# Performance work log

Hardware: AMD Instinct MI355X
Metric: run time of the kernel (lower is better)

The kernel has to match this reference:

```python
import jax, jax.numpy as jnp
import numpy as np

TEMPERATURE = 0.1
EPS = 1e-12  # matches torch F.normalize default eps


def setup_inputs() -> dict:
    key = jax.random.key(0)
    k1, k2 = jax.random.split(key)
    B, D = 4096, 512
    features1 = jax.random.normal(k1, (B, D), dtype=jnp.float32)
    features2 = jax.random.normal(k2, (B, D), dtype=jnp.float32)
    return {"features1": features1, "features2": features2}


def _l2_normalize(x, axis=1):
    norm = jnp.linalg.norm(x, axis=axis, keepdims=True)
    return x / jnp.maximum(norm, EPS)


def reference(features1, features2):
    B = features1.shape[0]
    f1 = _l2_normalize(features1)
    f2 = _l2_normalize(features2)
    features = jnp.concatenate([f1, f2], axis=0)  # (2B, D)
    sim = jnp.matmul(features, features.T) / TEMPERATURE  # (2B, 2B)
    # mask self-similarity on the diagonal with -inf
    diag = jnp.eye(2 * B, dtype=bool)
    sim = jnp.where(diag, -jnp.inf, sim)
    # positive pair labels: row i pairs with i+B (first half) / i-B (second half)
    labels = jnp.concatenate([jnp.arange(B) + B, jnp.arange(B)], axis=0)
    log_probs = jax.nn.log_softmax(sim, axis=-1)  # (2B, 2B)
    nll = -jnp.take_along_axis(log_probs, labels[:, None], axis=1)[:, 0]
    return jnp.mean(nll)
```

## Files before the change

kernel.cpp:

```cpp
#include <hip/hip_runtime.h>

#define NROWS 8192
#define HALF_N 4096
#define DIM 512
#define INV_T 10.0f
#define NRB 64
#define NBLOCKS 2080

typedef __attribute__((ext_vector_type(4))) float f32x4;
typedef __attribute__((ext_vector_type(2))) long long2v;

__device__ __forceinline__ void async16(const void* g, void* l) {
  __builtin_amdgcn_global_load_lds(
      (const __attribute__((address_space(1))) unsigned int*)g,
      (__attribute__((address_space(3))) unsigned int*)l, 16, 0, 0);
}

__global__ __launch_bounds__(256) void norm_cast_k(
    const float* __restrict__ f1, const float* __restrict__ f2,
    unsigned char* __restrict__ Fn, float* __restrict__ rowsum,
    float* __restrict__ out) {
  int wave = threadIdx.x >> 6;
  int lane = threadIdx.x & 63;
  int row = blockIdx.x * 4 + wave;
  const float* src = (row < HALF_N) ? (f1 + (size_t)row * DIM)
                                    : (f2 + (size_t)(row - HALF_N) * DIM);
  const float4* p = reinterpret_cast<const float4*>(src + lane * 8);
  float4 v0 = p[0];
  float4 v1 = p[1];
  float ss = v0.x*v0.x + v0.y*v0.y + v0.z*v0.z + v0.w*v0.w
           + v1.x*v1.x + v1.y*v1.y + v1.z*v1.z + v1.w*v1.w;
  #pragma unroll
  for (int off = 1; off < 64; off <<= 1) ss += __shfl_xor(ss, off);
  float scale = 1.0f / fmaxf(sqrtf(ss), 1e-12f);
  int lo = __builtin_amdgcn_cvt_pk_fp8_f32(v0.x * scale, v0.y * scale, 0, false);
  lo = __builtin_amdgcn_cvt_pk_fp8_f32(v0.z * scale, v0.w * scale, lo, true);
  int hi = __builtin_amdgcn_cvt_pk_fp8_f32(v1.x * scale, v1.y * scale, 0, false);
  hi = __builtin_amdgcn_cvt_pk_fp8_f32(v1.z * scale, v1.w * scale, hi, true);
  int u = lane & 7;
  int g = lane >> 3;
  int pos = 2 * (u & 3) + (u >> 2);
  *reinterpret_cast<int2*>(Fn + (size_t)row * DIM + g * 64 + pos * 8) =
      make_int2(lo, hi);
  if (lane == 0) rowsum[row] = 0.0f;
  if (blockIdx.x == 0 && threadIdx.x == 0) out[0] = 0.0f;
}

__global__ __launch_bounds__(256, 4) void sym_gemm_k(
    const unsigned char* __restrict__ Fn, float* __restrict__ rowsum,
    float* __restrict__ pairsim) {
  int bx = blockIdx.x;
  int gbx = (bx & 7) * (NBLOCKS / 8) + (bx >> 3);
  int rb = 0, rem = gbx;
  while (rem >= NRB - rb) { rem -= NRB - rb; ++rb; }
  const int cb = rb + rem;
  const int row0 = rb * 128, col0 = cb * 128;

  const int tid = threadIdx.x;
  const int wave = tid >> 6;
  const int lane = tid & 63;
  const int quad = lane >> 4;
  const int colid = lane & 15;
  const int wr0 = (wave >> 1) * 64;
  const int wc0 = (wave & 1) * 64;

  __shared__ __align__(16) unsigned char Alds[128 * 64];
  __shared__ __align__(16) unsigned char Blds[128 * 64];
  __shared__ float redrow[128];
  __shared__ float redcol[128];

  if (tid < 128) { redrow[tid] = 0.0f; redcol[tid] = 0.0f; }

  const unsigned char* srcA[2]; const unsigned char* srcB[2];
  unsigned char* dstA[2]; unsigned char* dstB[2];
  #pragma unroll
  for (int seg = 0; seg < 2; ++seg) {
    int inst = wave + seg * 4;
    int r = inst * 16 + (lane >> 2);
    int c = (lane & 3) ^ ((r >> 1) & 3);
    srcA[seg] = Fn + (size_t)(row0 + r) * DIM + c * 16;
    srcB[seg] = Fn + (size_t)(col0 + r) * DIM + c * 16;
    dstA[seg] = Alds + inst * 1024;
    dstB[seg] = Blds + inst * 1024;
  }

  const unsigned char* afp[4]; const unsigned char* bfp[4];
  #pragma unroll
  for (int t = 0; t < 4; ++t) {
    int ra = wr0 + t * 16 + colid;
    int rc = wc0 + t * 16 + colid;
    afp[t] = Alds + ra * 64 + ((quad ^ ((ra >> 1) & 3)) << 4);
    bfp[t] = Blds + rc * 64 + ((quad ^ ((rc >> 1) & 3)) << 4);
  }

  f32x4 acc[4][4];
  #pragma unroll
  for (int t = 0; t < 4; ++t)
    #pragma unroll
    for (int u = 0; u < 4; ++u) acc[t][u] = (f32x4){0.f, 0.f, 0.f, 0.f};

  for (int kc = 0; kc < 8; ++kc) {
    __syncthreads();
    const size_t ko = (size_t)kc * 64;
    #pragma unroll
    for (int seg = 0; seg < 2; ++seg) {
      async16(srcA[seg] + ko, dstA[seg]);
      async16(srcB[seg] + ko, dstB[seg]);
    }
    __syncthreads();

    long2v af[4], bf[4];
    #pragma unroll
    for (int t = 0; t < 4; ++t) af[t] = *reinterpret_cast<const long2v*>(afp[t]);
    #pragma unroll
    for (int u = 0; u < 4; ++u) bf[u] = *reinterpret_cast<const long2v*>(bfp[u]);
    #pragma unroll
    for (int s = 0; s < 2; ++s)
      #pragma unroll
      for (int t = 0; t < 4; ++t)
        #pragma unroll
        for (int u = 0; u < 4; ++u)
          acc[t][u] = __builtin_amdgcn_mfma_f32_16x16x32_fp8_fp8(
              af[t][s], bf[u][s], acc[t][u], 0, 0, 0);
  }

  float re[4][4];
  float ce[4];
  #pragma unroll
  for (int t = 0; t < 4; ++t)
    #pragma unroll
    for (int r = 0; r < 4; ++r) re[t][r] = 0.0f;
  #pragma unroll
  for (int u = 0; u < 4; ++u) ce[u] = 0.0f;

  #pragma unroll
  for (int t = 0; t < 4; ++t) {
    #pragma unroll
    for (int u = 0; u < 4; ++u) {
      f32x4 a = acc[t][u];
      const int gc = col0 + wc0 + u * 16 + colid;
      #pragma unroll
      for (int r = 0; r < 4; ++r) {
        int grow = row0 + wr0 + t * 16 + quad * 4 + r;
        float sim = a[r] * INV_T;
        float e = (gc > grow) ? __expf(sim) : 0.0f;
        re[t][r] += e;
        ce[u] += e;
        if (gc == grow + HALF_N && grow < HALF_N) {
          pairsim[grow] = sim;
          pairsim[gc] = sim;
        }
      }
    }
  }

  #pragma unroll
  for (int t = 0; t < 4; ++t)
    #pragma unroll
    for (int r = 0; r < 4; ++r) {
      float v = re[t][r];
      v += __shfl_xor(v, 1); v += __shfl_xor(v, 2);
      v += __shfl_xor(v, 4); v += __shfl_xor(v, 8);
      if (colid == 0) atomicAdd(&redrow[wr0 + t * 16 + quad * 4 + r], v);
    }
  #pragma unroll
  for (int u = 0; u < 4; ++u) {
    float v = ce[u];
    v += __shfl_xor(v, 16); v += __shfl_xor(v, 32);
    if (lane < 16) atomicAdd(&redcol[wc0 + u * 16 + colid], v);
  }
  __syncthreads();
  if (tid < 128) atomicAdd(&rowsum[row0 + tid], redrow[tid]);
  else           atomicAdd(&rowsum[col0 + tid - 128], redcol[tid - 128]);
}

__global__ __launch_bounds__(256) void finalize_k(
    const float* __restrict__ rowsum, const float* __restrict__ pairsim,
    float* __restrict__ out) {
  int i = blockIdx.x * 256 + threadIdx.x;
  float local = logf(rowsum[i]) - pairsim[i];
  #pragma unroll
  for (int off = 1; off < 64; off <<= 1) local += __shfl_xor(local, off);
  if ((threadIdx.x & 63) == 0)
    atomicAdd(out, local * (1.0f / (float)NROWS));
}

extern "C" void kernel_launch(void* const* d_in, const int* in_sizes, int n_in,
                              void* d_out, int out_size, void* d_ws, size_t ws_size,
                              hipStream_t stream) {
  const float* f1 = (const float*)d_in[0];
  const float* f2 = (const float*)d_in[1];
  unsigned char* Fn = (unsigned char*)d_ws;
  float* rowsum = (float*)((char*)d_ws + (size_t)NROWS * DIM);
  float* pairsim = rowsum + NROWS;
  float* out = (float*)d_out;

  norm_cast_k<<<NROWS / 4, 256, 0, stream>>>(f1, f2, Fn, rowsum, out);
  sym_gemm_k<<<NBLOCKS, 256, 0, stream>>>(Fn, rowsum, pairsim);
  finalize_k<<<NROWS / 256, 256, 0, stream>>>(rowsum, pairsim, out);
}
```

Baseline: 104.4 us.

## Load A operand directly from global in MFMA-fragment layout, bypass LDS

The normalize kernel now writes a second FP8 copy of the features in a fragment-major layout, so each lane can load its A-operand MFMA fragment directly from global memory with one 16-byte load. The GEMM drops the A tile from LDS, halving shared-memory staging and LDS reads, and issues the A global loads before the barrier. Occupancy is lowered to 3 blocks per SM in launch bounds. The cost is an extra 4 MB workspace write and A loads that now go to global/L2 without reuse across waves.

```diff
diff --git a/kernel.cpp b/kernel.cpp
--- a/kernel.cpp
+++ b/kernel.cpp
@@ -18,8 +18,8 @@
 
 __global__ __launch_bounds__(256) void norm_cast_k(
     const float* __restrict__ f1, const float* __restrict__ f2,
-    unsigned char* __restrict__ Fn, float* __restrict__ rowsum,
-    float* __restrict__ out) {
+    unsigned char* __restrict__ Fa, unsigned char* __restrict__ Fb,
+    float* __restrict__ rowsum, float* __restrict__ out) {
   int wave = threadIdx.x >> 6;
   int lane = threadIdx.x & 63;
   int row = blockIdx.x * 4 + wave;
@@ -37,18 +37,22 @@
   lo = __builtin_amdgcn_cvt_pk_fp8_f32(v0.z * scale, v0.w * scale, lo, true);
   int hi = __builtin_amdgcn_cvt_pk_fp8_f32(v1.x * scale, v1.y * scale, 0, false);
   hi = __builtin_amdgcn_cvt_pk_fp8_f32(v1.z * scale, v1.w * scale, hi, true);
+  int2 val = make_int2(lo, hi);
   int u = lane & 7;
   int g = lane >> 3;
   int pos = 2 * (u & 3) + (u >> 2);
-  *reinterpret_cast<int2*>(Fn + (size_t)row * DIM + g * 64 + pos * 8) =
-      make_int2(lo, hi);
+  *reinterpret_cast<int2*>(Fb + (size_t)row * DIM + g * 64 + pos * 8) = val;
+  int chunk = g * 4 + (u & 3);
+  int slot = u >> 2;
+  *reinterpret_cast<int2*>(Fa + (size_t)(row >> 4) * 8192 + chunk * 256 +
+                           (row & 15) * 16 + slot * 8) = val;
   if (lane == 0) rowsum[row] = 0.0f;
   if (blockIdx.x == 0 && threadIdx.x == 0) out[0] = 0.0f;
 }
 
-__global__ __launch_bounds__(256, 4) void sym_gemm_k(
-    const unsigned char* __restrict__ Fn, float* __restrict__ rowsum,
-    float* __restrict__ pairsim) {
+__global__ __launch_bounds__(256, 3) void sym_gemm_k(
+    const unsigned char* __restrict__ Fa, const unsigned char* __restrict__ Fb,
+    float* __restrict__ rowsum, float* __restrict__ pairsim) {
   int bx = blockIdx.x;
   int gbx = (bx & 7) * (NBLOCKS / 8) + (bx >> 3);
   int rb = 0, rem = gbx;
@@ -64,32 +68,32 @@
   const int wr0 = (wave >> 1) * 64;
   const int wc0 = (wave & 1) * 64;
 
-  __shared__ __align__(16) unsigned char Alds[128 * 64];
   __shared__ __align__(16) unsigned char Blds[128 * 64];
   __shared__ float redrow[128];
   __shared__ float redcol[128];
 
   if (tid < 128) { redrow[tid] = 0.0f; redcol[tid] = 0.0f; }
 
-  const unsigned char* srcA[2]; const unsigned char* srcB[2];
-  unsigned char* dstA[2]; unsigned char* dstB[2];
+  const unsigned char* srcB[2]; unsigned char* dstB[2];
   #pragma unroll
   for (int seg = 0; seg < 2; ++seg) {
     int inst = wave + seg * 4;
     int r = inst * 16 + (lane >> 2);
     int c = (lane & 3) ^ ((r >> 1) & 3);
-    srcA[seg] = Fn + (size_t)(row0 + r) * DIM + c * 16;
-    srcB[seg] = Fn + (size_t)(col0 + r) * DIM + c * 16;
-    dstA[seg] = Alds + inst * 1024;
+    srcB[seg] = Fb + (size_t)(col0 + r) * DIM + c * 16;
     dstB[seg] = Blds + inst * 1024;
   }
 
-  const unsigned char* afp[4]; const unsigned char* bfp[4];
+  const unsigned char* agp[4];
+  #pragma unroll
+  for (int t = 0; t < 4; ++t)
+    agp[t] = Fa + (size_t)((row0 + wr0 + t * 16) >> 4) * 8192 +
+             quad * 256 + colid * 16;
+
+  const unsigned char* bfp[4];
   #pragma unroll
   for (int t = 0; t < 4; ++t) {
-    int ra = wr0 + t * 16 + colid;
     int rc = wc0 + t * 16 + colid;
-    afp[t] = Alds + ra * 64 + ((quad ^ ((ra >> 1) & 3)) << 4);
     bfp[t] = Blds + rc * 64 + ((quad ^ ((rc >> 1) & 3)) << 4);
   }
 
@@ -103,15 +107,15 @@
     __syncthreads();
     const size_t ko = (size_t)kc * 64;
     #pragma unroll
-    for (int seg = 0; seg < 2; ++seg) {
-      async16(srcA[seg] + ko, dstA[seg]);
+    for (int seg = 0; seg < 2; ++seg)
       async16(srcB[seg] + ko, dstB[seg]);
-    }
+    long2v af[4];
+    #pragma unroll
+    for (int t = 0; t < 4; ++t)
+      af[t] = *reinterpret_cast<const long2v*>(agp[t] + kc * 1024);
     __syncthreads();
 
-    long2v af[4], bf[4];
-    #pragma unroll
-    for (int t = 0; t < 4; ++t) af[t] = *reinterpret_cast<const long2v*>(afp[t]);
+    long2v bf[4];
     #pragma unroll
     for (int u = 0; u < 4; ++u) bf[u] = *reinterpret_cast<const long2v*>(bfp[u]);
     #pragma unroll
@@ -190,12 +194,13 @@
                               hipStream_t stream) {
   const float* f1 = (const float*)d_in[0];
   const float* f2 = (const float*)d_in[1];
-  unsigned char* Fn = (unsigned char*)d_ws;
-  float* rowsum = (float*)((char*)d_ws + (size_t)NROWS * DIM);
+  unsigned char* Fa = (unsigned char*)d_ws;
+  unsigned char* Fb = Fa + (size_t)NROWS * DIM;
+  float* rowsum = (float*)(Fb + (size_t)NROWS * DIM);
   float* pairsim = rowsum + NROWS;
   float* out = (float*)d_out;
 
-  norm_cast_k<<<NROWS / 4, 256, 0, stream>>>(f1, f2, Fn, rowsum, out);
-  sym_gemm_k<<<NBLOCKS, 256, 0, stream>>>(Fn, rowsum, pairsim);
+  norm_cast_k<<<NROWS / 4, 256, 0, stream>>>(f1, f2, Fa, Fb, rowsum, out);
+  sym_gemm_k<<<NBLOCKS, 256, 0, stream>>>(Fa, Fb, rowsum, pairsim);
   finalize_k<<<NROWS / 256, 256, 0, stream>>>(rowsum, pairsim, out);
 }
```

New measurement: 104.2 us, median of 2. Within noise of the previous version (-0.2%).
